# Performance work log

Hardware: AMD Instinct MI355X
Metric: run time of the kernel (lower is better)

## Reference

```python
import jax, jax.numpy as jnp
import numpy as np

BN_EPS = 1e-5


def knn_idx(x, k):
    # x: (B, N, C) -> (B, N, k) indices of k nearest neighbors (incl. self),
    # DGCNN style: topk of negative squared distance.
    inner = jnp.einsum('bnc,bmc->bnm', x, x)
    sq = jnp.sum(x * x, axis=-1)
    neg_dist = 2.0 * inner - sq[:, :, None] - sq[:, None, :]
    _, idx = jax.lax.top_k(neg_dist, k)
    return idx


def edge_conv(x, W, b, gamma, beta, k):
    # x: (B, N, C); W: (O, 2C). One DGCNN EdgeConv block:
    # knn gather -> concat(nbr - x, x) -> conv1x1 -> BN(batch stats) -> GELU -> max over k.
    idx = knn_idx(x, k)                                   # (B, N, k)
    nbr = jax.vmap(lambda f, i: f[i])(x, idx)             # (B, N, k, C)
    ctr = jnp.broadcast_to(x[:, :, None, :], nbr.shape)
    feat = jnp.concatenate([nbr - ctr, ctr], axis=-1)     # (B, N, k, 2C)
    y = jnp.einsum('bnkc,oc->bnko', feat, W) + b          # conv 1x1
    mean = jnp.mean(y, axis=(0, 1, 2))
    var = jnp.var(y, axis=(0, 1, 2))
    y = (y - mean) * jax.lax.rsqrt(var + BN_EPS) * gamma + beta
    y = jax.nn.gelu(y, approximate=False)                 # torch nn.GELU default (erf)
    return jnp.max(y, axis=2)                             # (B, N, O)


def setup_inputs() -> dict:
    key = jax.random.key(0)
    ks = jax.random.split(key, 8)
    bs, ch, n_patches, n_samples = 4, 6, 32, 256
    dims_in = [12, 32, 64, 128, 256]
    dims_out = [16, 32, 64, 128, 256]
    inp = {'x': jax.random.normal(ks[0], (bs, ch, n_patches, n_samples), dtype=jnp.float32)}
    for i, (ci, co) in enumerate(zip(dims_in, dims_out), start=1):
        wk = jax.random.fold_in(ks[1], i)
        scale = 1.0 / np.sqrt(ci)
        inp[f'W{i}'] = (jax.random.normal(wk, (co, ci), dtype=jnp.float32) * scale)
        inp[f'b{i}'] = jnp.zeros((co,), dtype=jnp.float32)
        inp[f'g{i}'] = jnp.ones((co,), dtype=jnp.float32)
        inp[f'bt{i}'] = jnp.zeros((co,), dtype=jnp.float32)
    inp['k'] = 16
    return inp


def reference(x, W1, b1, g1, bt1, W2, b2, g2, bt2, W3, b3, g3, bt3,
              W4, b4, g4, bt4, W5, b5, g5, bt5, k):
    bs, ch, n_patches, n_samples = x.shape
    # (bs, ch, P, S) -> (bs*P, S, ch)  [channels-last point clouds]
    h = x.transpose(0, 2, 3, 1).reshape(bs * n_patches, n_samples, ch)
    h = edge_conv(h, W1, b1, g1, bt1, k)
    h = edge_conv(h, W2, b2, g2, bt2, k)
    h = edge_conv(h, W3, b3, g3, bt3, k)
    h = edge_conv(h, W4, b4, g4, bt4, k)
    h = edge_conv(h, W5, b5, g5, bt5, k)      # (bs*P, S, dim)
    dim = h.shape[-1]
    h = h.reshape(bs, n_patches, n_samples, dim)
    return h.transpose(0, 3, 1, 2)            # (bs, dim, n_patches, n_samples)
```

## Files before the change

kernel.cpp:

```cpp
#include <hip/hip_runtime.h>
#include <cmath>

#define NPTS 256
#define TOTPTS 32768
#define KNB 16

static const size_t OFF_HA   = 0;
static const size_t OFF_HB   = 4194304;
static const size_t OFF_UZ   = 6291456;
static const size_t OFF_YMAX = 23068672;
static const size_t OFF_YMIN = 31457280;
static const size_t OFF_IDX  = 39845888;
static const size_t OFF_VT   = 40370176;
static const size_t OFF_SUMS = 40458240;

__device__ __forceinline__ float gelu_erf(float v) {
  return 0.5f * v * (1.0f + erff(v * 0.70710678118654752f));
}

__global__ __launch_bounds__(256) void prep_kernel(
    const float* __restrict__ x, float* __restrict__ h0,
    const float* __restrict__ W1, const float* __restrict__ W2, const float* __restrict__ W3,
    const float* __restrict__ W4, const float* __restrict__ W5,
    float* __restrict__ Vt, double* __restrict__ sums) {
  const int stride = gridDim.x * blockDim.x;
  const int tid0 = blockIdx.x * blockDim.x + threadIdx.x;
  for (int id = tid0; id < 196608; id += stride) {
    int ch = id % 6;
    int r  = id / 6;
    int s  = r & 255;
    int p  = (r >> 8) & 31;
    int bs = r >> 13;
    h0[id] = x[(((size_t)(bs * 6 + ch) * 32 + p) << 8) + s];
  }
  for (int id = tid0; id < 87232; id += stride) {
    const float* W; int K, N2, base;
    if (id < 192)        { W = W1; K = 6;   N2 = 32;  base = 0; }
    else if (id < 1216)  { W = W2; K = 16;  N2 = 64;  base = 192; }
    else if (id < 5312)  { W = W3; K = 32;  N2 = 128; base = 1216; }
    else if (id < 21696) { W = W4; K = 64;  N2 = 256; base = 5312; }
    else                 { W = W5; K = 128; N2 = 512; base = 21696; }
    int e = id - base;
    int c = e / N2;
    int j = e - c * N2;
    int O = N2 >> 1;
    Vt[id] = (j < O) ? W[j * 2 * K + c] : W[(j - O) * 2 * K + K + c];
  }
  for (int id = tid0; id < 992; id += stride) sums[id] = 0.0;
}

template<int C>
__global__ __launch_bounds__(256) void sq_kernel(const float* __restrict__ h,
                                                 double* __restrict__ sqd) {
  const int n = blockIdx.x * 256 + threadIdx.x;
  const float* p = h + (size_t)n * C;
  double q0 = 0.0, q1 = 0.0;
  #pragma unroll
  for (int c = 0; c + 1 < C; c += 2) {
    q0 = fma((double)p[c],   (double)p[c],   q0);
    q1 = fma((double)p[c+1], (double)p[c+1], q1);
  }
  #pragma unroll
  for (int c = C & ~1; c < C; ++c) q0 = fma((double)p[c], (double)p[c], q0);
  sqd[n] = q0 + q1;
}

template<int K>
__global__ __launch_bounds__(256) void dist_kernel(const float* __restrict__ h,
                                                   const double* __restrict__ sqd,
                                                   double* __restrict__ nd) {
  constexpr int KC = (K < 32) ? K : 32;
  __shared__ __align__(16) float As[KC * 68];
  __shared__ __align__(16) float Bs[KC * 68];
  const int cloud = blockIdx.x >> 4;
  const int tile  = blockIdx.x & 15;
  const int i0 = (tile >> 2) * 64;
  const int j0 = (tile & 3) * 64;
  const float* hb = h + (size_t)cloud * NPTS * K;
  const int tid = threadIdx.x;
  const int mm = (tid & 15) * 4;
  const int jj = (tid >> 4) * 4;
  double acc[4][4] = {{0.0}};
  for (int k0 = 0; k0 < K; k0 += KC) {
    for (int e = tid; e < 64 * KC; e += 256) {
      int am = e / KC, ac = e - am * KC;
      As[ac * 68 + am] = hb[(size_t)(i0 + am) * K + k0 + ac];
    }
    for (int e = tid; e < 64 * KC; e += 256) {
      int bm = e / KC, bc = e - bm * KC;
      Bs[bc * 68 + bm] = hb[(size_t)(j0 + bm) * K + k0 + bc];
    }
    __syncthreads();
    #pragma unroll
    for (int c = 0; c < KC; ++c) {
      float4 av = *(const float4*)(As + c * 68 + mm);
      float4 bv = *(const float4*)(Bs + c * 68 + jj);
      double a0 = (double)av.x, a1 = (double)av.y, a2 = (double)av.z, a3 = (double)av.w;
      double b0 = (double)bv.x, b1 = (double)bv.y, b2 = (double)bv.z, b3 = (double)bv.w;
      acc[0][0] = fma(a0, b0, acc[0][0]);
      acc[0][1] = fma(a0, b1, acc[0][1]);
      acc[0][2] = fma(a0, b2, acc[0][2]);
      acc[0][3] = fma(a0, b3, acc[0][3]);
      acc[1][0] = fma(a1, b0, acc[1][0]);
      acc[1][1] = fma(a1, b1, acc[1][1]);
      acc[1][2] = fma(a1, b2, acc[1][2]);
      acc[1][3] = fma(a1, b3, acc[1][3]);
      acc[2][0] = fma(a2, b0, acc[2][0]);
      acc[2][1] = fma(a2, b1, acc[2][1]);
      acc[2][2] = fma(a2, b2, acc[2][2]);
      acc[2][3] = fma(a2, b3, acc[2][3]);
      acc[3][0] = fma(a3, b0, acc[3][0]);
      acc[3][1] = fma(a3, b1, acc[3][1]);
      acc[3][2] = fma(a3, b2, acc[3][2]);
      acc[3][3] = fma(a3, b3, acc[3][3]);
    }
    __syncthreads();
  }
  double sqi[4], sqj[4];
  #pragma unroll
  for (int r = 0; r < 4; ++r) sqi[r] = sqd[cloud * NPTS + i0 + mm + r];
  #pragma unroll
  for (int s = 0; s < 4; ++s) sqj[s] = sqd[cloud * NPTS + j0 + jj + s];
  double* orow = nd + (size_t)cloud * NPTS * NPTS;
  #pragma unroll
  for (int r = 0; r < 4; ++r) {
    double v0 = 2.0 * acc[r][0] - sqi[r] - sqj[0];
    double v1 = 2.0 * acc[r][1] - sqi[r] - sqj[1];
    double v2 = 2.0 * acc[r][2] - sqi[r] - sqj[2];
    double v3 = 2.0 * acc[r][3] - sqi[r] - sqj[3];
    double* p = orow + (size_t)(i0 + mm + r) * NPTS + j0 + jj;
    *(double2*)(p)     = make_double2(v0, v1);
    *(double2*)(p + 2) = make_double2(v2, v3);
  }
}

__global__ __launch_bounds__(256) void topk_merge2_kernel(const double* __restrict__ nd,
                                                          int* __restrict__ idxout) {
  const unsigned long long FULL = 0xFFFFFFFFFFFFFFFFull;
  const int wid  = threadIdx.x >> 6;
  const int lane = threadIdx.x & 63;
  const int half = lane >> 5;
  const int sub  = lane & 31;
  const int rowAB = blockIdx.x * 16 + wid * 4 + half;
  const int rowCD = blockIdx.x * 16 + wid * 4 + 2 + half;
  const double* rp1 = nd + (size_t)rowAB * NPTS + 8 * sub;
  const double* rp2 = nd + (size_t)rowCD * NPTS + 8 * sub;
  const unsigned cb = 8u * (unsigned)sub;

  #define MK(P, Q) ((((unsigned long long)__double_as_longlong(P)) & ~0xFFull) | (cb + (Q)))
  double2 t0 = *(const double2*)(rp1);
  double2 t1 = *(const double2*)(rp1 + 2);
  double2 t2 = *(const double2*)(rp1 + 4);
  double2 t3 = *(const double2*)(rp1 + 6);
  unsigned long long a0 = MK(t0.x, 0u), a1 = MK(t0.y, 1u), a2 = MK(t1.x, 2u), a3 = MK(t1.y, 3u);
  unsigned long long a4 = MK(t2.x, 4u), a5 = MK(t2.y, 5u), a6 = MK(t3.x, 6u), a7 = MK(t3.y, 7u);
  t0 = *(const double2*)(rp2);
  t1 = *(const double2*)(rp2 + 2);
  t2 = *(const double2*)(rp2 + 4);
  t3 = *(const double2*)(rp2 + 6);
  unsigned long long b0 = MK(t0.x, 0u), b1 = MK(t0.y, 1u), b2 = MK(t1.x, 2u), b3 = MK(t1.y, 3u);
  unsigned long long b4 = MK(t2.x, 4u), b5 = MK(t2.y, 5u), b6 = MK(t3.x, 6u), b7 = MK(t3.y, 7u);
  #undef MK

  #define CE(X, Y) { unsigned long long lo_ = (X < Y) ? X : Y; \
                     unsigned long long hi_ = (X < Y) ? Y : X; X = lo_; Y = hi_; }
  #define SORT8(v0,v1,v2,v3,v4,v5,v6,v7) \
    CE(v0,v1) CE(v2,v3) CE(v4,v5) CE(v6,v7) \
    CE(v0,v2) CE(v1,v3) CE(v4,v6) CE(v5,v7) \
    CE(v1,v2) CE(v5,v6) \
    CE(v0,v4) CE(v1,v5) CE(v2,v6) CE(v3,v7) \
    CE(v2,v4) CE(v3,v5) \
    CE(v1,v2) CE(v3,v4) CE(v5,v6)
  SORT8(a0,a1,a2,a3,a4,a5,a6,a7)
  SORT8(b0,b1,b2,b3,b4,b5,b6,b7)
  #undef SORT8
  #undef CE

  int keep1 = 0, keep2 = 0;
  for (int round = 0; round < KNB; ++round) {
    unsigned long long m1 = a0, m2 = b0, o;
    o = __shfl_xor(m1, 16); m1 = (o < m1) ? o : m1;
    o = __shfl_xor(m2, 16); m2 = (o < m2) ? o : m2;
    o = __shfl_xor(m1, 8);  m1 = (o < m1) ? o : m1;
    o = __shfl_xor(m2, 8);  m2 = (o < m2) ? o : m2;
    o = __shfl_xor(m1, 4);  m1 = (o < m1) ? o : m1;
    o = __shfl_xor(m2, 4);  m2 = (o < m2) ? o : m2;
    o = __shfl_xor(m1, 2);  m1 = (o < m1) ? o : m1;
    o = __shfl_xor(m2, 2);  m2 = (o < m2) ? o : m2;
    o = __shfl_xor(m1, 1);  m1 = (o < m1) ? o : m1;
    o = __shfl_xor(m2, 1);  m2 = (o < m2) ? o : m2;
    const int col1 = (int)(m1 & 0xFFull);
    const int col2 = (int)(m2 & 0xFFull);
    if ((col1 >> 3) == sub) {
      a0 = a1; a1 = a2; a2 = a3; a3 = a4; a4 = a5; a5 = a6; a6 = a7; a7 = FULL;
    }
    if ((col2 >> 3) == sub) {
      b0 = b1; b1 = b2; b2 = b3; b3 = b4; b4 = b5; b5 = b6; b6 = b7; b7 = FULL;
    }
    if (sub == round) { keep1 = col1; keep2 = col2; }
  }
  if (sub < KNB) {
    idxout[(size_t)rowAB * KNB + sub] = (rowAB & ~(NPTS - 1)) + keep1;
    idxout[(size_t)rowCD * KNB + sub] = (rowCD & ~(NPTS - 1)) + keep2;
  }
}

template<int K, int N2>
__global__ __launch_bounds__(256) void gemm_uz_kernel(const float* __restrict__ h,
                                                      const float* __restrict__ Vt,
                                                      float* __restrict__ UZ) {
  constexpr int KC = 32;
  constexpr int NBLK = (N2 + 63) / 64;
  __shared__ __align__(16) float As[KC * 68];
  __shared__ __align__(16) float Bs[KC * 68];
  const int m0 = (int)(blockIdx.x / NBLK) * 64;
  const int n0 = (int)(blockIdx.x % NBLK) * 64;
  const int tid = threadIdx.x;
  const int mm = (tid & 15) * 4;
  const int jj = (tid >> 4) * 4;
  float acc[4][4] = {{0.f}};
  for (int k0 = 0; k0 < K; k0 += KC) {
    #pragma unroll
    for (int e = tid; e < 64 * KC; e += 256) {
      int am = e / KC, ac = e - am * KC;
      float v = 0.f;
      if (k0 + ac < K) v = h[(size_t)(m0 + am) * K + k0 + ac];
      As[ac * 68 + am] = v;
    }
    #pragma unroll
    for (int e = tid; e < KC * 64; e += 256) {
      int bj = e & 63, bc = e >> 6;
      float v = 0.f;
      if (k0 + bc < K && n0 + bj < N2) v = Vt[(size_t)(k0 + bc) * N2 + n0 + bj];
      Bs[bc * 68 + bj] = v;
    }
    __syncthreads();
    #pragma unroll
    for (int c = 0; c < KC; ++c) {
      float4 av = *(const float4*)(As + c * 68 + mm);
      float4 bv = *(const float4*)(Bs + c * 68 + jj);
      acc[0][0] = fmaf(av.x, bv.x, acc[0][0]);
      acc[0][1] = fmaf(av.x, bv.y, acc[0][1]);
      acc[0][2] = fmaf(av.x, bv.z, acc[0][2]);
      acc[0][3] = fmaf(av.x, bv.w, acc[0][3]);
      acc[1][0] = fmaf(av.y, bv.x, acc[1][0]);
      acc[1][1] = fmaf(av.y, bv.y, acc[1][1]);
      acc[1][2] = fmaf(av.y, bv.z, acc[1][2]);
      acc[1][3] = fmaf(av.y, bv.w, acc[1][3]);
      acc[2][0] = fmaf(av.z, bv.x, acc[2][0]);
      acc[2][1] = fmaf(av.z, bv.y, acc[2][1]);
      acc[2][2] = fmaf(av.z, bv.z, acc[2][2]);
      acc[2][3] = fmaf(av.z, bv.w, acc[2][3]);
      acc[3][0] = fmaf(av.w, bv.x, acc[3][0]);
      acc[3][1] = fmaf(av.w, bv.y, acc[3][1]);
      acc[3][2] = fmaf(av.w, bv.z, acc[3][2]);
      acc[3][3] = fmaf(av.w, bv.w, acc[3][3]);
    }
    __syncthreads();
  }
  if (n0 + jj < N2) {
    #pragma unroll
    for (int i = 0; i < 4; ++i) {
      float4 v = make_float4(acc[i][0], acc[i][1], acc[i][2], acc[i][3]);
      *(float4*)(UZ + (size_t)(m0 + mm + i) * N2 + n0 + jj) = v;
    }
  }
}

template<int K, int N2>
__global__ __launch_bounds__(256) void gemm_big_kernel(const float* __restrict__ h,
                                                       const float* __restrict__ Vt,
                                                       float* __restrict__ UZ) {
  constexpr int KC = 32;
  constexpr int PAD = 132;
  constexpr int NBLK = N2 / 128;
  __shared__ __align__(16) float As[KC * PAD];
  __shared__ __align__(16) float Bs[KC * PAD];
  const int m0 = (int)(blockIdx.x / NBLK) * 128;
  const int n0 = (int)(blockIdx.x % NBLK) * 128;
  const int tid = threadIdx.x;
  const int ra = (tid & 15) * 4;
  const int ca = (tid >> 4) * 4;
  float acc[8][8];
  #pragma unroll
  for (int i = 0; i < 8; ++i)
    #pragma unroll
    for (int j = 0; j < 8; ++j) acc[i][j] = 0.f;

  for (int k0 = 0; k0 < K; k0 += KC) {
    #pragma unroll
    for (int q = 0; q < 4; ++q) {
      int idx = tid + 256 * q;
      int am = idx >> 3;
      int aq = idx & 7;
      float4 v = *(const float4*)(h + (size_t)(m0 + am) * K + k0 + 4 * aq);
      As[(4 * aq + 0) * PAD + am] = v.x;
      As[(4 * aq + 1) * PAD + am] = v.y;
      As[(4 * aq + 2) * PAD + am] = v.z;
      As[(4 * aq + 3) * PAD + am] = v.w;
    }
    #pragma unroll
    for (int q = 0; q < 4; ++q) {
      int idx = tid + 256 * q;
      int bk = idx >> 5;
      int bq = idx & 31;
      *(float4*)(Bs + bk * PAD + 4 * bq) =
          *(const float4*)(Vt + (size_t)(k0 + bk) * N2 + n0 + 4 * bq);
    }
    __syncthreads();
    #pragma unroll
    for (int cc = 0; cc < KC; ++cc) {
      float4 a0 = *(const float4*)(As + cc * PAD + ra);
      float4 a1 = *(const float4*)(As + cc * PAD + 64 + ra);
      float4 b0 = *(const float4*)(Bs + cc * PAD + ca);
      float4 b1 = *(const float4*)(Bs + cc * PAD + 64 + ca);
      float av[8] = {a0.x, a0.y, a0.z, a0.w, a1.x, a1.y, a1.z, a1.w};
      float bv[8] = {b0.x, b0.y, b0.z, b0.w, b1.x, b1.y, b1.z, b1.w};
      #pragma unroll
      for (int i = 0; i < 8; ++i)
        #pragma unroll
        for (int j = 0; j < 8; ++j)
          acc[i][j] = fmaf(av[i], bv[j], acc[i][j]);
    }
    __syncthreads();
  }
  #pragma unroll
  for (int i = 0; i < 8; ++i) {
    int row = m0 + ((i < 4) ? (ra + i) : (64 + ra + (i - 4)));
    float4 v0 = make_float4(acc[i][0], acc[i][1], acc[i][2], acc[i][3]);
    float4 v1 = make_float4(acc[i][4], acc[i][5], acc[i][6], acc[i][7]);
    *(float4*)(UZ + (size_t)row * N2 + n0 + ca) = v0;
    *(float4*)(UZ + (size_t)row * N2 + n0 + 64 + ca) = v1;
  }
}

template<int O, int GRID>
__global__ __launch_bounds__(256) void combine_kernel(const float* __restrict__ UZ,
    const int* __restrict__ idx, const float* __restrict__ bias,
    float* __restrict__ ymax, float* __restrict__ ymin, double* __restrict__ partials) {
  constexpr int TPP = O / 4;
  constexpr int PPI = 256 / TPP;
  constexpr int PPB = TOTPTS / GRID;
  constexpr int ITERS = PPB / PPI;
  static_assert(ITERS >= 1, "grid too large for this O");
  constexpr int BPC = GRID / 128;
  __shared__ double red[256];
  const int tid = threadIdx.x;
  const int oc  = tid % TPP;
  const int sub = tid / TPP;
  const int x    = blockIdx.x & 7;
  const int slot = blockIdx.x >> 3;
  const int c    = x + 8 * (slot / BPC);
  const int w    = slot % BPC;
  const int base = c * NPTS + w * PPB;
  const float4* UZ4 = (const float4*)UZ;
  float4* ymx4 = (float4*)ymax;
  float4* ymn4 = (float4*)ymin;
  const float4 b4 = ((const float4*)bias)[oc];
  double a1x = 0.0, a1y = 0.0, a1z = 0.0, a1w = 0.0;
  double a2x = 0.0, a2y = 0.0, a2z = 0.0, a2w = 0.0;
  for (int it = 0; it < ITERS; ++it) {
    int n = base + it * PPI + sub;
    const int* ip = idx + (size_t)n * KNB;
    float4 un = UZ4[(size_t)n * (O / 2) + oc];
    float4 zn = UZ4[(size_t)n * (O / 2) + O / 4 + oc];
    float4 w4 = make_float4(zn.x - un.x + b4.x, zn.y - un.y + b4.y,
                            zn.z - un.z + b4.z, zn.w - un.w + b4.w);
    float4 mx = make_float4(-INFINITY, -INFINITY, -INFINITY, -INFINITY);
    float4 mn = make_float4(INFINITY, INFINITY, INFINITY, INFINITY);
    float4 s1 = make_float4(0.f, 0.f, 0.f, 0.f);
    float4 s2 = make_float4(0.f, 0.f, 0.f, 0.f);
    #pragma unroll
    for (int kk = 0; kk < KNB; ++kk) {
      int j = ip[kk];
      float4 uv = UZ4[(size_t)j * (O / 2) + oc];
      mx.x = fmaxf(mx.x, uv.x); mx.y = fmaxf(mx.y, uv.y);
      mx.z = fmaxf(mx.z, uv.z); mx.w = fmaxf(mx.w, uv.w);
      mn.x = fminf(mn.x, uv.x); mn.y = fminf(mn.y, uv.y);
      mn.z = fminf(mn.z, uv.z); mn.w = fminf(mn.w, uv.w);
      s1.x += uv.x; s1.y += uv.y; s1.z += uv.z; s1.w += uv.w;
      s2.x = fmaf(uv.x, uv.x, s2.x); s2.y = fmaf(uv.y, uv.y, s2.y);
      s2.z = fmaf(uv.z, uv.z, s2.z); s2.w = fmaf(uv.w, uv.w, s2.w);
    }
    ymx4[(size_t)n * (O / 4) + oc] = make_float4(mx.x + w4.x, mx.y + w4.y, mx.z + w4.z, mx.w + w4.w);
    ymn4[(size_t)n * (O / 4) + oc] = make_float4(mn.x + w4.x, mn.y + w4.y, mn.z + w4.z, mn.w + w4.w);
    a1x += (double)(s1.x + 16.f * w4.x);
    a1y += (double)(s1.y + 16.f * w4.y);
    a1z += (double)(s1.z + 16.f * w4.z);
    a1w += (double)(s1.w + 16.f * w4.w);
    a2x += (double)(s2.x + 2.f * w4.x * s1.x + 16.f * (w4.x * w4.x));
    a2y += (double)(s2.y + 2.f * w4.y * s1.y + 16.f * (w4.y * w4.y));
    a2z += (double)(s2.z + 2.f * w4.z * s1.z + 16.f * (w4.z * w4.z));
    a2w += (double)(s2.w + 2.f * w4.w * s1.w + 16.f * (w4.w * w4.w));
  }
  #define REDUCE_ONE(VAL, CH_OFF)                                        \
    red[tid] = (VAL);                                                    \
    __syncthreads();                                                     \
    if (tid < TPP) {                                                     \
      double t = 0.0;                                                    \
      _Pragma("unroll")                                                  \
      for (int q = 0; q < PPI; ++q) t += red[q * TPP + tid];             \
      partials[(size_t)((CH_OFF) + 4 * tid) * GRID + blockIdx.x] = t;    \
    }                                                                    \
    __syncthreads();
  REDUCE_ONE(a1x, 0)
  REDUCE_ONE(a1y, 1)
  REDUCE_ONE(a1z, 2)
  REDUCE_ONE(a1w, 3)
  REDUCE_ONE(a2x, O + 0)
  REDUCE_ONE(a2y, O + 1)
  REDUCE_ONE(a2z, O + 2)
  REDUCE_ONE(a2w, O + 3)
  #undef REDUCE_ONE
}

template<int NB>
__global__ __launch_bounds__(256) void reduce_sums_kernel(const double* __restrict__ part,
                                                          double* __restrict__ sums) {
  __shared__ double red[256];
  const int ch = blockIdx.x;
  const double* p = part + (size_t)ch * NB;
  double t = 0.0;
  for (int i = threadIdx.x; i < NB; i += 256) t += p[i];
  red[threadIdx.x] = t;
  __syncthreads();
  #pragma unroll
  for (int s = 128; s > 0; s >>= 1) {
    if (threadIdx.x < s) red[threadIdx.x] += red[threadIdx.x + s];
    __syncthreads();
  }
  if (threadIdx.x == 0) sums[ch] = red[0];
}

template<int O>
__global__ __launch_bounds__(256) void apply_kernel(const float* __restrict__ ymax,
    const float* __restrict__ ymin, const double* __restrict__ sums,
    const float* __restrict__ g, const float* __restrict__ bt, float* __restrict__ hout) {
  const int tid = blockIdx.x * 256 + threadIdx.x;
  const int o = tid & (O - 1);
  double m = sums[o] * (1.0 / 524288.0);
  double v = fma(-m, m, sums[O + o] * (1.0 / 524288.0));
  float A = g[o] / sqrtf((float)v + 1e-5f);
  float Cc = fmaf(-(float)m, A, bt[o]);
  float r1 = gelu_erf(fmaf(A, ymax[tid], Cc));
  float r2 = gelu_erf(fmaf(A, ymin[tid], Cc));
  hout[tid] = fmaxf(r1, r2);
}

__global__ __launch_bounds__(256) void apply_final_kernel(const float* __restrict__ ymax,
    const float* __restrict__ ymin, const double* __restrict__ sums,
    const float* __restrict__ g, const float* __restrict__ bt, float* __restrict__ out) {
  constexpr int O = 256;
  __shared__ float tile[64 * 65];
  const int bo = blockIdx.x & 3;
  const int bn = blockIdx.x >> 2;
  const int n0 = bn * 64, o0 = bo * 64;
  const int lane = threadIdx.x & 63;
  const int grp = threadIdx.x >> 6;
  {
    const int oc = o0 + lane;
    double m = sums[oc] * (1.0 / 524288.0);
    double v = fma(-m, m, sums[O + oc] * (1.0 / 524288.0));
    float A = g[oc] / sqrtf((float)v + 1e-5f);
    float Cc = fmaf(-(float)m, A, bt[oc]);
    #pragma unroll
    for (int q = 0; q < 16; ++q) {
      int r = grp * 16 + q;
      size_t src = (size_t)(n0 + r) * O + oc;
      float r1 = gelu_erf(fmaf(A, ymax[src], Cc));
      float r2 = gelu_erf(fmaf(A, ymin[src], Cc));
      tile[r * 65 + lane] = fmaxf(r1, r2);
    }
  }
  __syncthreads();
  const int s0 = n0 & 255;
  const int p  = (n0 >> 8) & 31;
  const int bs = n0 >> 13;
  size_t basei = ((size_t)(bs * 256 + o0) * 32 + p) * 256 + s0;
  #pragma unroll
  for (int q = 0; q < 16; ++q) {
    int c = grp * 16 + q;
    out[basei + (size_t)c * 8192 + lane] = tile[lane * 65 + c];
  }
}

extern "C" void kernel_launch(void* const* d_in, const int* in_sizes, int n_in,
                              void* d_out, int out_size, void* d_ws, size_t ws_size,
                              hipStream_t stream) {
  (void)in_sizes; (void)n_in; (void)out_size; (void)ws_size;
  const float* x   = (const float*)d_in[0];
  const float* W1  = (const float*)d_in[1];
  const float* b1  = (const float*)d_in[2];
  const float* g1  = (const float*)d_in[3];
  const float* bt1 = (const float*)d_in[4];
  const float* W2  = (const float*)d_in[5];
  const float* b2  = (const float*)d_in[6];
  const float* g2  = (const float*)d_in[7];
  const float* bt2 = (const float*)d_in[8];
  const float* W3  = (const float*)d_in[9];
  const float* b3  = (const float*)d_in[10];
  const float* g3  = (const float*)d_in[11];
  const float* bt3 = (const float*)d_in[12];
  const float* W4  = (const float*)d_in[13];
  const float* b4  = (const float*)d_in[14];
  const float* g4  = (const float*)d_in[15];
  const float* bt4 = (const float*)d_in[16];
  const float* W5  = (const float*)d_in[17];
  const float* b5  = (const float*)d_in[18];
  const float* g5  = (const float*)d_in[19];
  const float* bt5 = (const float*)d_in[20];

  float* ws    = (float*)d_ws;
  float* hA    = ws + OFF_HA;
  float* hB    = ws + OFF_HB;
  float* UZ    = ws + OFF_UZ;
  float* ymx   = ws + OFF_YMAX;
  float* ymn   = ws + OFF_YMIN;
  int*   idxb  = (int*)(ws + OFF_IDX);
  float* Vt    = ws + OFF_VT;
  double* sums = (double*)(ws + OFF_SUMS);
  double* nd   = (double*)UZ;
  double* sqd  = (double*)ymx;
  double* partA = (double*)hA;
  double* partB = (double*)hB;

  prep_kernel<<<256, 256, 0, stream>>>(x, hA, W1, W2, W3, W4, W5, Vt, sums);

  sq_kernel<6><<<128, 256, 0, stream>>>(hA, sqd);
  dist_kernel<6><<<2048, 256, 0, stream>>>(hA, sqd, nd);
  topk_merge2_kernel<<<2048, 256, 0, stream>>>(nd, idxb);
  gemm_uz_kernel<6, 32><<<512, 256, 0, stream>>>(hA, Vt + 0, UZ);
  combine_kernel<16, 512><<<512, 256, 0, stream>>>(UZ, idxb, b1, ymx, ymn, partA);
  reduce_sums_kernel<512><<<32, 256, 0, stream>>>(partA, sums + 0);
  apply_kernel<16><<<2048, 256, 0, stream>>>(ymx, ymn, sums + 0, g1, bt1, hB);

  sq_kernel<16><<<128, 256, 0, stream>>>(hB, sqd);
  dist_kernel<16><<<2048, 256, 0, stream>>>(hB, sqd, nd);
  topk_merge2_kernel<<<2048, 256, 0, stream>>>(nd, idxb);
  gemm_uz_kernel<16, 64><<<512, 256, 0, stream>>>(hB, Vt + 192, UZ);
  combine_kernel<32, 1024><<<1024, 256, 0, stream>>>(UZ, idxb, b2, ymx, ymn, partB);
  reduce_sums_kernel<1024><<<64, 256, 0, stream>>>(partB, sums + 32);
  apply_kernel<32><<<4096, 256, 0, stream>>>(ymx, ymn, sums + 32, g2, bt2, hA);

  sq_kernel<32><<<128, 256, 0, stream>>>(hA, sqd);
  dist_kernel<32><<<2048, 256, 0, stream>>>(hA, sqd, nd);
  topk_merge2_kernel<<<2048, 256, 0, stream>>>(nd, idxb);
  gemm_big_kernel<32, 128><<<256, 256, 0, stream>>>(hA, Vt + 1216, UZ);
  combine_kernel<64, 2048><<<2048, 256, 0, stream>>>(UZ, idxb, b3, ymx, ymn, partA);
  reduce_sums_kernel<2048><<<128, 256, 0, stream>>>(partA, sums + 96);
  apply_kernel<64><<<8192, 256, 0, stream>>>(ymx, ymn, sums + 96, g3, bt3, hB);

  sq_kernel<64><<<128, 256, 0, stream>>>(hB, sqd);
  dist_kernel<64><<<2048, 256, 0, stream>>>(hB, sqd, nd);
  topk_merge2_kernel<<<2048, 256, 0, stream>>>(nd, idxb);
  gemm_big_kernel<64, 256><<<512, 256, 0, stream>>>(hB, Vt + 5312, UZ);
  combine_kernel<128, 2048><<<2048, 256, 0, stream>>>(UZ, idxb, b4, ymx, ymn, partB);
  reduce_sums_kernel<2048><<<256, 256, 0, stream>>>(partB, sums + 224);
  apply_kernel<128><<<16384, 256, 0, stream>>>(ymx, ymn, sums + 224, g4, bt4, hA);

  sq_kernel<128><<<128, 256, 0, stream>>>(hA, sqd);
  dist_kernel<128><<<2048, 256, 0, stream>>>(hA, sqd, nd);
  topk_merge2_kernel<<<2048, 256, 0, stream>>>(nd, idxb);
  gemm_big_kernel<128, 512><<<1024, 256, 0, stream>>>(hA, Vt + 21696, UZ);
  combine_kernel<256, 2048><<<2048, 256, 0, stream>>>(UZ, idxb, b5, ymx, ymn, partA);
  reduce_sums_kernel<2048><<<512, 256, 0, stream>>>(partA, sums + 480);
  apply_final_kernel<<<2048, 256, 0, stream>>>(ymx, ymn, sums + 480, g5, bt5, (float*)d_out);
}
```

Baseline: 708.4 us.

## Fuse pairwise-distance GEMM with top-k selection in shared memory

Merges the distance kernel and the top-k kernel into one kernel per layer. Each block computes 32 rows by all 256 columns of the negative distance matrix in fp64, packs the keys into shared memory and runs the existing warp-shuffle top-16 selection from there. This removes the write and re-read of the 256x256 fp64 distance matrix per cloud through global memory, plus one launch per layer. In exchange it uses about 66KB of shared memory per block, which limits occupancy, and the column tile is reloaded twice per block.

```diff
diff --git a/kernel.cpp b/kernel.cpp
--- a/kernel.cpp
+++ b/kernel.cpp
@@ -66,142 +66,137 @@
 }
 
 template<int K>
-__global__ __launch_bounds__(256) void dist_kernel(const float* __restrict__ h,
-                                                   const double* __restrict__ sqd,
-                                                   double* __restrict__ nd) {
-  constexpr int KC = (K < 32) ? K : 32;
-  __shared__ __align__(16) float As[KC * 68];
-  __shared__ __align__(16) float Bs[KC * 68];
-  const int cloud = blockIdx.x >> 4;
-  const int tile  = blockIdx.x & 15;
-  const int i0 = (tile >> 2) * 64;
-  const int j0 = (tile & 3) * 64;
+__global__ __launch_bounds__(256) void knn_fused_kernel(const float* __restrict__ h,
+                                                        const double* __restrict__ sqd,
+                                                        int* __restrict__ idxout) {
+  constexpr int KC = (K < 16) ? K : 16;
+  __shared__ unsigned long long keys[32 * 257];
+  __shared__ __align__(16) float As[KC * 36];
+  __shared__ __align__(16) float Bs[KC * 132];
+  const int cloud = blockIdx.x >> 3;
+  const int i0 = (blockIdx.x & 7) * 32;
   const float* hb = h + (size_t)cloud * NPTS * K;
   const int tid = threadIdx.x;
-  const int mm = (tid & 15) * 4;
-  const int jj = (tid >> 4) * 4;
-  double acc[4][4] = {{0.0}};
-  for (int k0 = 0; k0 < K; k0 += KC) {
-    for (int e = tid; e < 64 * KC; e += 256) {
-      int am = e / KC, ac = e - am * KC;
-      As[ac * 68 + am] = hb[(size_t)(i0 + am) * K + k0 + ac];
-    }
-    for (int e = tid; e < 64 * KC; e += 256) {
-      int bm = e / KC, bc = e - bm * KC;
-      Bs[bc * 68 + bm] = hb[(size_t)(j0 + bm) * K + k0 + bc];
-    }
-    __syncthreads();
-    #pragma unroll
-    for (int c = 0; c < KC; ++c) {
-      float4 av = *(const float4*)(As + c * 68 + mm);
-      float4 bv = *(const float4*)(Bs + c * 68 + jj);
-      double a0 = (double)av.x, a1 = (double)av.y, a2 = (double)av.z, a3 = (double)av.w;
-      double b0 = (double)bv.x, b1 = (double)bv.y, b2 = (double)bv.z, b3 = (double)bv.w;
-      acc[0][0] = fma(a0, b0, acc[0][0]);
-      acc[0][1] = fma(a0, b1, acc[0][1]);
-      acc[0][2] = fma(a0, b2, acc[0][2]);
-      acc[0][3] = fma(a0, b3, acc[0][3]);
-      acc[1][0] = fma(a1, b0, acc[1][0]);
-      acc[1][1] = fma(a1, b1, acc[1][1]);
-      acc[1][2] = fma(a1, b2, acc[1][2]);
-      acc[1][3] = fma(a1, b3, acc[1][3]);
-      acc[2][0] = fma(a2, b0, acc[2][0]);
-      acc[2][1] = fma(a2, b1, acc[2][1]);
-      acc[2][2] = fma(a2, b2, acc[2][2]);
-      acc[2][3] = fma(a2, b3, acc[2][3]);
-      acc[3][0] = fma(a3, b0, acc[3][0]);
-      acc[3][1] = fma(a3, b1, acc[3][1]);
-      acc[3][2] = fma(a3, b2, acc[3][2]);
-      acc[3][3] = fma(a3, b3, acc[3][3]);
-    }
-    __syncthreads();
-  }
-  double sqi[4], sqj[4];
+  const int mm = (tid & 7) * 4;
+  const int jj = (tid >> 3) * 4;
+
+  double sqi[4];
   #pragma unroll
   for (int r = 0; r < 4; ++r) sqi[r] = sqd[cloud * NPTS + i0 + mm + r];
-  #pragma unroll
-  for (int s = 0; s < 4; ++s) sqj[s] = sqd[cloud * NPTS + j0 + jj + s];
-  double* orow = nd + (size_t)cloud * NPTS * NPTS;
-  #pragma unroll
-  for (int r = 0; r < 4; ++r) {
-    double v0 = 2.0 * acc[r][0] - sqi[r] - sqj[0];
-    double v1 = 2.0 * acc[r][1] - sqi[r] - sqj[1];
-    double v2 = 2.0 * acc[r][2] - sqi[r] - sqj[2];
-    double v3 = 2.0 * acc[r][3] - sqi[r] - sqj[3];
-    double* p = orow + (size_t)(i0 + mm + r) * NPTS + j0 + jj;
-    *(double2*)(p)     = make_double2(v0, v1);
-    *(double2*)(p + 2) = make_double2(v2, v3);
-  }
-}
-
-__global__ __launch_bounds__(256) void topk_merge2_kernel(const double* __restrict__ nd,
-                                                          int* __restrict__ idxout) {
+
+  for (int jh = 0; jh < 2; ++jh) {
+    const int j0 = jh * 128;
+    double acc[4][4] = {{0.0}};
+    for (int k0 = 0; k0 < K; k0 += KC) {
+      for (int e = tid; e < 32 * KC; e += 256) {
+        int am = e / KC, ac = e - am * KC;
+        As[ac * 36 + am] = hb[(size_t)(i0 + am) * K + k0 + ac];
+      }
+      for (int e = tid; e < 128 * KC; e += 256) {
+        int bm = e / KC, bc = e - bm * KC;
+        Bs[bc * 132 + bm] = hb[(size_t)(j0 + bm) * K + k0 + bc];
+      }
+      __syncthreads();
+      #pragma unroll
+      for (int c = 0; c < KC; ++c) {
+        float4 av = *(const float4*)(As + c * 36 + mm);
+        float4 bv = *(const float4*)(Bs + c * 132 + jj);
+        double a0 = (double)av.x, a1 = (double)av.y, a2 = (double)av.z, a3 = (double)av.w;
+        double b0 = (double)bv.x, b1 = (double)bv.y, b2 = (double)bv.z, b3 = (double)bv.w;
+        acc[0][0] = fma(a0, b0, acc[0][0]);
+        acc[0][1] = fma(a0, b1, acc[0][1]);
+        acc[0][2] = fma(a0, b2, acc[0][2]);
+        acc[0][3] = fma(a0, b3, acc[0][3]);
+        acc[1][0] = fma(a1, b0, acc[1][0]);
+        acc[1][1] = fma(a1, b1, acc[1][1]);
+        acc[1][2] = fma(a1, b2, acc[1][2]);
+        acc[1][3] = fma(a1, b3, acc[1][3]);
+        acc[2][0] = fma(a2, b0, acc[2][0]);
+        acc[2][1] = fma(a2, b1, acc[2][1]);
+        acc[2][2] = fma(a2, b2, acc[2][2]);
+        acc[2][3] = fma(a2, b3, acc[2][3]);
+        acc[3][0] = fma(a3, b0, acc[3][0]);
+        acc[3][1] = fma(a3, b1, acc[3][1]);
+        acc[3][2] = fma(a3, b2, acc[3][2]);
+        acc[3][3] = fma(a3, b3, acc[3][3]);
+      }
+      __syncthreads();
+    }
+    double sqj[4];
+    #pragma unroll
+    for (int s = 0; s < 4; ++s) sqj[s] = sqd[cloud * NPTS + j0 + jj + s];
+    #pragma unroll
+    for (int r = 0; r < 4; ++r) {
+      #pragma unroll
+      for (int s = 0; s < 4; ++s) {
+        double v = 2.0 * acc[r][s] - sqi[r] - sqj[s];
+        int col = j0 + jj + s;
+        keys[(mm + r) * 257 + col] =
+            (((unsigned long long)__double_as_longlong(v)) & ~0xFFull) |
+            (unsigned long long)col;
+      }
+    }
+  }
+  __syncthreads();
+
   const unsigned long long FULL = 0xFFFFFFFFFFFFFFFFull;
-  const int wid  = threadIdx.x >> 6;
-  const int lane = threadIdx.x & 63;
+  const int wid  = tid >> 6;
+  const int lane = tid & 63;
   const int half = lane >> 5;
   const int sub  = lane & 31;
-  const int rowAB = blockIdx.x * 16 + wid * 4 + half;
-  const int rowCD = blockIdx.x * 16 + wid * 4 + 2 + half;
-  const double* rp1 = nd + (size_t)rowAB * NPTS + 8 * sub;
-  const double* rp2 = nd + (size_t)rowCD * NPTS + 8 * sub;
-  const unsigned cb = 8u * (unsigned)sub;
-
-  #define MK(P, Q) ((((unsigned long long)__double_as_longlong(P)) & ~0xFFull) | (cb + (Q)))
-  double2 t0 = *(const double2*)(rp1);
-  double2 t1 = *(const double2*)(rp1 + 2);
-  double2 t2 = *(const double2*)(rp1 + 4);
-  double2 t3 = *(const double2*)(rp1 + 6);
-  unsigned long long a0 = MK(t0.x, 0u), a1 = MK(t0.y, 1u), a2 = MK(t1.x, 2u), a3 = MK(t1.y, 3u);
-  unsigned long long a4 = MK(t2.x, 4u), a5 = MK(t2.y, 5u), a6 = MK(t3.x, 6u), a7 = MK(t3.y, 7u);
-  t0 = *(const double2*)(rp2);
-  t1 = *(const double2*)(rp2 + 2);
-  t2 = *(const double2*)(rp2 + 4);
-  t3 = *(const double2*)(rp2 + 6);
-  unsigned long long b0 = MK(t0.x, 0u), b1 = MK(t0.y, 1u), b2 = MK(t1.x, 2u), b3 = MK(t1.y, 3u);
-  unsigned long long b4 = MK(t2.x, 4u), b5 = MK(t2.y, 5u), b6 = MK(t3.x, 6u), b7 = MK(t3.y, 7u);
-  #undef MK
-
-  #define CE(X, Y) { unsigned long long lo_ = (X < Y) ? X : Y; \
-                     unsigned long long hi_ = (X < Y) ? Y : X; X = lo_; Y = hi_; }
-  #define SORT8(v0,v1,v2,v3,v4,v5,v6,v7) \
-    CE(v0,v1) CE(v2,v3) CE(v4,v5) CE(v6,v7) \
-    CE(v0,v2) CE(v1,v3) CE(v4,v6) CE(v5,v7) \
-    CE(v1,v2) CE(v5,v6) \
-    CE(v0,v4) CE(v1,v5) CE(v2,v6) CE(v3,v7) \
-    CE(v2,v4) CE(v3,v5) \
-    CE(v1,v2) CE(v3,v4) CE(v5,v6)
-  SORT8(a0,a1,a2,a3,a4,a5,a6,a7)
-  SORT8(b0,b1,b2,b3,b4,b5,b6,b7)
-  #undef SORT8
-  #undef CE
-
-  int keep1 = 0, keep2 = 0;
-  for (int round = 0; round < KNB; ++round) {
-    unsigned long long m1 = a0, m2 = b0, o;
-    o = __shfl_xor(m1, 16); m1 = (o < m1) ? o : m1;
-    o = __shfl_xor(m2, 16); m2 = (o < m2) ? o : m2;
-    o = __shfl_xor(m1, 8);  m1 = (o < m1) ? o : m1;
-    o = __shfl_xor(m2, 8);  m2 = (o < m2) ? o : m2;
-    o = __shfl_xor(m1, 4);  m1 = (o < m1) ? o : m1;
-    o = __shfl_xor(m2, 4);  m2 = (o < m2) ? o : m2;
-    o = __shfl_xor(m1, 2);  m1 = (o < m1) ? o : m1;
-    o = __shfl_xor(m2, 2);  m2 = (o < m2) ? o : m2;
-    o = __shfl_xor(m1, 1);  m1 = (o < m1) ? o : m1;
-    o = __shfl_xor(m2, 1);  m2 = (o < m2) ? o : m2;
-    const int col1 = (int)(m1 & 0xFFull);
-    const int col2 = (int)(m2 & 0xFFull);
-    if ((col1 >> 3) == sub) {
-      a0 = a1; a1 = a2; a2 = a3; a3 = a4; a4 = a5; a5 = a6; a6 = a7; a7 = FULL;
-    }
-    if ((col2 >> 3) == sub) {
-      b0 = b1; b1 = b2; b2 = b3; b3 = b4; b4 = b5; b5 = b6; b6 = b7; b7 = FULL;
-    }
-    if (sub == round) { keep1 = col1; keep2 = col2; }
-  }
-  if (sub < KNB) {
-    idxout[(size_t)rowAB * KNB + sub] = (rowAB & ~(NPTS - 1)) + keep1;
-    idxout[(size_t)rowCD * KNB + sub] = (rowCD & ~(NPTS - 1)) + keep2;
+  for (int p = 0; p < 2; ++p) {
+    const int rA = p * 16 + wid * 4 + half;
+    const int rC = rA + 2;
+    const unsigned long long* rp1 = keys + rA * 257 + 8 * sub;
+    const unsigned long long* rp2 = keys + rC * 257 + 8 * sub;
+    unsigned long long a0 = rp1[0], a1 = rp1[1], a2 = rp1[2], a3 = rp1[3];
+    unsigned long long a4 = rp1[4], a5 = rp1[5], a6 = rp1[6], a7 = rp1[7];
+    unsigned long long b0 = rp2[0], b1 = rp2[1], b2 = rp2[2], b3 = rp2[3];
+    unsigned long long b4 = rp2[4], b5 = rp2[5], b6 = rp2[6], b7 = rp2[7];
+
+    #define CE(X, Y) { unsigned long long lo_ = (X < Y) ? X : Y; \
+                       unsigned long long hi_ = (X < Y) ? Y : X; X = lo_; Y = hi_; }
+    #define SORT8(v0,v1,v2,v3,v4,v5,v6,v7) \
+      CE(v0,v1) CE(v2,v3) CE(v4,v5) CE(v6,v7) \
+      CE(v0,v2) CE(v1,v3) CE(v4,v6) CE(v5,v7) \
+      CE(v1,v2) CE(v5,v6) \
+      CE(v0,v4) CE(v1,v5) CE(v2,v6) CE(v3,v7) \
+      CE(v2,v4) CE(v3,v5) \
+      CE(v1,v2) CE(v3,v4) CE(v5,v6)
+    SORT8(a0,a1,a2,a3,a4,a5,a6,a7)
+    SORT8(b0,b1,b2,b3,b4,b5,b6,b7)
+    #undef SORT8
+    #undef CE
+
+    int keep1 = 0, keep2 = 0;
+    for (int round = 0; round < KNB; ++round) {
+      unsigned long long m1 = a0, m2 = b0, o;
+      o = __shfl_xor(m1, 16); m1 = (o < m1) ? o : m1;
+      o = __shfl_xor(m2, 16); m2 = (o < m2) ? o : m2;
+      o = __shfl_xor(m1, 8);  m1 = (o < m1) ? o : m1;
+      o = __shfl_xor(m2, 8);  m2 = (o < m2) ? o : m2;
+      o = __shfl_xor(m1, 4);  m1 = (o < m1) ? o : m1;
+      o = __shfl_xor(m2, 4);  m2 = (o < m2) ? o : m2;
+      o = __shfl_xor(m1, 2);  m1 = (o < m1) ? o : m1;
+      o = __shfl_xor(m2, 2);  m2 = (o < m2) ? o : m2;
+      o = __shfl_xor(m1, 1);  m1 = (o < m1) ? o : m1;
+      o = __shfl_xor(m2, 1);  m2 = (o < m2) ? o : m2;
+      const int col1 = (int)(m1 & 0xFFull);
+      const int col2 = (int)(m2 & 0xFFull);
+      if ((col1 >> 3) == sub) {
+        a0 = a1; a1 = a2; a2 = a3; a3 = a4; a4 = a5; a5 = a6; a6 = a7; a7 = FULL;
+      }
+      if ((col2 >> 3) == sub) {
+        b0 = b1; b1 = b2; b2 = b3; b3 = b4; b4 = b5; b5 = b6; b6 = b7; b7 = FULL;
+      }
+      if (sub == round) { keep1 = col1; keep2 = col2; }
+    }
+    if (sub < KNB) {
+      const int growA = cloud * NPTS + i0 + rA;
+      const int growC = cloud * NPTS + i0 + rC;
+      idxout[(size_t)growA * KNB + sub] = cloud * NPTS + keep1;
+      idxout[(size_t)growC * KNB + sub] = cloud * NPTS + keep2;
+    }
   }
 }
 
@@ -519,7 +514,6 @@
   int*   idxb  = (int*)(ws + OFF_IDX);
   float* Vt    = ws + OFF_VT;
   double* sums = (double*)(ws + OFF_SUMS);
-  double* nd   = (double*)UZ;
   double* sqd  = (double*)ymx;
   double* partA = (double*)hA;
   double* partB = (double*)hB;
@@ -527,40 +521,35 @@
   prep_kernel<<<256, 256, 0, stream>>>(x, hA, W1, W2, W3, W4, W5, Vt, sums);
 
   sq_kernel<6><<<128, 256, 0, stream>>>(hA, sqd);
-  dist_kernel<6><<<2048, 256, 0, stream>>>(hA, sqd, nd);
-  topk_merge2_kernel<<<2048, 256, 0, stream>>>(nd, idxb);
+  knn_fused_kernel<6><<<1024, 256, 0, stream>>>(hA, sqd, idxb);
   gemm_uz_kernel<6, 32><<<512, 256, 0, stream>>>(hA, Vt + 0, UZ);
   combine_kernel<16, 512><<<512, 256, 0, stream>>>(UZ, idxb, b1, ymx, ymn, partA);
   reduce_sums_kernel<512><<<32, 256, 0, stream>>>(partA, sums + 0);
   apply_kernel<16><<<2048, 256, 0, stream>>>(ymx, ymn, sums + 0, g1, bt1, hB);
 
   sq_kernel<16><<<128, 256, 0, stream>>>(hB, sqd);
-  dist_kernel<16><<<2048, 256, 0, stream>>>(hB, sqd, nd);
-  topk_merge2_kernel<<<2048, 256, 0, stream>>>(nd, idxb);
+  knn_fused_kernel<16><<<1024, 256, 0, stream>>>(hB, sqd, idxb);
   gemm_uz_kernel<16, 64><<<512, 256, 0, stream>>>(hB, Vt + 192, UZ);
   combine_kernel<32, 1024><<<1024, 256, 0, stream>>>(UZ, idxb, b2, ymx, ymn, partB);
   reduce_sums_kernel<1024><<<64, 256, 0, stream>>>(partB, sums + 32);
   apply_kernel<32><<<4096, 256, 0, stream>>>(ymx, ymn, sums + 32, g2, bt2, hA);
 
   sq_kernel<32><<<128, 256, 0, stream>>>(hA, sqd);
-  dist_kernel<32><<<2048, 256, 0, stream>>>(hA, sqd, nd);
-  topk_merge2_kernel<<<2048, 256, 0, stream>>>(nd, idxb);
+  knn_fused_kernel<32><<<1024, 256, 0, stream>>>(hA, sqd, idxb);
   gemm_big_kernel<32, 128><<<256, 256, 0, stream>>>(hA, Vt + 1216, UZ);
   combine_kernel<64, 2048><<<2048, 256, 0, stream>>>(UZ, idxb, b3, ymx, ymn, partA);
   reduce_sums_kernel<2048><<<128, 256, 0, stream>>>(partA, sums + 96);
   apply_kernel<64><<<8192, 256, 0, stream>>>(ymx, ymn, sums + 96, g3, bt3, hB);
 
   sq_kernel<64><<<128, 256, 0, stream>>>(hB, sqd);
-  dist_kernel<64><<<2048, 256, 0, stream>>>(hB, sqd, nd);
-  topk_merge2_kernel<<<2048, 256, 0, stream>>>(nd, idxb);
+  knn_fused_kernel<64><<<1024, 256, 0, stream>>>(hB, sqd, idxb);
   gemm_big_kernel<64, 256><<<512, 256, 0, stream>>>(hB, Vt + 5312, UZ);
   combine_kernel<128, 2048><<<2048, 256, 0, stream>>>(UZ, idxb, b4, ymx, ymn, partB);
   reduce_sums_kernel<2048><<<256, 256, 0, stream>>>(partB, sums + 224);
   apply_kernel<128><<<16384, 256, 0, stream>>>(ymx, ymn, sums + 224, g4, bt4, hA);
 
   sq_kernel<128><<<128, 256, 0, stream>>>(hA, sqd);
-  dist_kernel<128><<<2048, 256, 0, stream>>>(hA, sqd, nd);
-  topk_merge2_kernel<<<2048, 256, 0, stream>>>(nd, idxb);
+  knn_fused_kernel<128><<<1024, 256, 0, stream>>>(hA, sqd, idxb);
   gemm_big_kernel<128, 512><<<1024, 256, 0, stream>>>(hA, Vt + 21696, UZ);
   combine_kernel<256, 2048><<<2048, 256, 0, stream>>>(UZ, idxb, b5, ymx, ymn, partA);
   reduce_sums_kernel<2048><<<512, 256, 0, stream>>>(partA, sums + 480);
```

Measured after the change: 784.7 us. +10.8%, slower.

## Exploit distance symmetry and overlap per-layer GEMM with kNN on a second stream

Applied to the files above, without the earlier changes.

The distance kernel now computes only the upper-triangular 64x64 tiles of each cloud's 256x256 distance matrix (10 of 16 tiles) and mirrors the off-diagonal tiles by writing them transposed. Blocks are mapped so that consecutive block IDs go to different XCDs. Each layer's UZ GEMM now runs on a second stream, overlapping the sq/dist/top-k chain and joined with events before combine. Buffers are reassigned so that the concurrent kernels do not alias: nd goes into the ymx region and the sq buffers into the free h buffer. The trade-offs are uncoalesced transposed stores, event overhead, and correctness that depends on buffer lifetimes and on the static second stream.

```diff
diff --git a/kernel.cpp b/kernel.cpp
--- a/kernel.cpp
+++ b/kernel.cpp
@@ -66,16 +66,20 @@
 }
 
 template<int K>
-__global__ __launch_bounds__(256) void dist_kernel(const float* __restrict__ h,
-                                                   const double* __restrict__ sqd,
-                                                   double* __restrict__ nd) {
+__global__ __launch_bounds__(256) void dist_sym_kernel(const float* __restrict__ h,
+                                                       const double* __restrict__ sqd,
+                                                       double* __restrict__ nd) {
   constexpr int KC = (K < 32) ? K : 32;
   __shared__ __align__(16) float As[KC * 68];
   __shared__ __align__(16) float Bs[KC * 68];
-  const int cloud = blockIdx.x >> 4;
-  const int tile  = blockIdx.x & 15;
-  const int i0 = (tile >> 2) * 64;
-  const int j0 = (tile & 3) * 64;
+  const int xcd  = blockIdx.x & 7;
+  const int t    = blockIdx.x >> 3;
+  const int cloud = xcd + 8 * (t / 10);
+  const int p    = t % 10;
+  const int ti   = (p < 4) ? 0 : ((p < 7) ? 1 : ((p < 9) ? 2 : 3));
+  const int tj   = p - ((ti == 0) ? 0 : ((ti == 1) ? 3 : ((ti == 2) ? 5 : 6)));
+  const int i0 = ti * 64;
+  const int j0 = tj * 64;
   const float* hb = h + (size_t)cloud * NPTS * K;
   const int tid = threadIdx.x;
   const int mm = (tid & 15) * 4;
@@ -128,9 +132,21 @@
     double v1 = 2.0 * acc[r][1] - sqi[r] - sqj[1];
     double v2 = 2.0 * acc[r][2] - sqi[r] - sqj[2];
     double v3 = 2.0 * acc[r][3] - sqi[r] - sqj[3];
-    double* p = orow + (size_t)(i0 + mm + r) * NPTS + j0 + jj;
-    *(double2*)(p)     = make_double2(v0, v1);
-    *(double2*)(p + 2) = make_double2(v2, v3);
+    double* pw = orow + (size_t)(i0 + mm + r) * NPTS + j0 + jj;
+    *(double2*)(pw)     = make_double2(v0, v1);
+    *(double2*)(pw + 2) = make_double2(v2, v3);
+  }
+  if (i0 != j0) {
+    #pragma unroll
+    for (int s = 0; s < 4; ++s) {
+      double m0 = 2.0 * acc[0][s] - sqj[s] - sqi[0];
+      double m1 = 2.0 * acc[1][s] - sqj[s] - sqi[1];
+      double m2 = 2.0 * acc[2][s] - sqj[s] - sqi[2];
+      double m3 = 2.0 * acc[3][s] - sqj[s] - sqi[3];
+      double* pT = orow + (size_t)(j0 + jj + s) * NPTS + i0 + mm;
+      *(double2*)(pT)     = make_double2(m0, m1);
+      *(double2*)(pT + 2) = make_double2(m2, m3);
+    }
   }
 }
 
@@ -519,50 +535,77 @@
   int*   idxb  = (int*)(ws + OFF_IDX);
   float* Vt    = ws + OFF_VT;
   double* sums = (double*)(ws + OFF_SUMS);
-  double* nd   = (double*)UZ;
-  double* sqd  = (double*)ymx;
+  double* nd   = (double*)ymx;
+  double* sqA  = (double*)hA;
+  double* sqB  = (double*)hB;
   double* partA = (double*)hA;
   double* partB = (double*)hB;
 
+  static hipStream_t s2 = nullptr;
+  static hipEvent_t evF[5], evJ[5];
+  if (s2 == nullptr) {
+    hipStreamCreateWithFlags(&s2, hipStreamNonBlocking);
+    for (int i = 0; i < 5; ++i) {
+      hipEventCreateWithFlags(&evF[i], hipEventDisableTiming);
+      hipEventCreateWithFlags(&evJ[i], hipEventDisableTiming);
+    }
+  }
+
+  #define FORK(l)  hipEventRecord(evF[l], stream); hipStreamWaitEvent(s2, evF[l], 0);
+  #define JOIN(l)  hipEventRecord(evJ[l], s2);     hipStreamWaitEvent(stream, evJ[l], 0);
+
   prep_kernel<<<256, 256, 0, stream>>>(x, hA, W1, W2, W3, W4, W5, Vt, sums);
 
-  sq_kernel<6><<<128, 256, 0, stream>>>(hA, sqd);
-  dist_kernel<6><<<2048, 256, 0, stream>>>(hA, sqd, nd);
+  FORK(0)
+  gemm_uz_kernel<6, 32><<<512, 256, 0, s2>>>(hA, Vt + 0, UZ);
+  sq_kernel<6><<<128, 256, 0, stream>>>(hA, sqB);
+  dist_sym_kernel<6><<<1280, 256, 0, stream>>>(hA, sqB, nd);
   topk_merge2_kernel<<<2048, 256, 0, stream>>>(nd, idxb);
-  gemm_uz_kernel<6, 32><<<512, 256, 0, stream>>>(hA, Vt + 0, UZ);
+  JOIN(0)
   combine_kernel<16, 512><<<512, 256, 0, stream>>>(UZ, idxb, b1, ymx, ymn, partA);
   reduce_sums_kernel<512><<<32, 256, 0, stream>>>(partA, sums + 0);
   apply_kernel<16><<<2048, 256, 0, stream>>>(ymx, ymn, sums + 0, g1, bt1, hB);
 
-  sq_kernel<16><<<128, 256, 0, stream>>>(hB, sqd);
-  dist_kernel<16><<<2048, 256, 0, stream>>>(hB, sqd, nd);
+  FORK(1)
+  gemm_uz_kernel<16, 64><<<512, 256, 0, s2>>>(hB, Vt + 192, UZ);
+  sq_kernel<16><<<128, 256, 0, stream>>>(hB, sqA);
+  dist_sym_kernel<16><<<1280, 256, 0, stream>>>(hB, sqA, nd);
   topk_merge2_kernel<<<2048, 256, 0, stream>>>(nd, idxb);
-  gemm_uz_kernel<16, 64><<<512, 256, 0, stream>>>(hB, Vt + 192, UZ);
+  JOIN(1)
   combine_kernel<32, 1024><<<1024, 256, 0, stream>>>(UZ, idxb, b2, ymx, ymn, partB);
   reduce_sums_kernel<1024><<<64, 256, 0, stream>>>(partB, sums + 32);
   apply_kernel<32><<<4096, 256, 0, stream>>>(ymx, ymn, sums + 32, g2, bt2, hA);
 
-  sq_kernel<32><<<128, 256, 0, stream>>>(hA, sqd);
-  dist_kernel<32><<<2048, 256, 0, stream>>>(hA, sqd, nd);
+  FORK(2)
+  gemm_big_kernel<32, 128><<<256, 256, 0, s2>>>(hA, Vt + 1216, UZ);
+  sq_kernel<32><<<128, 256, 0, stream>>>(hA, sqB);
+  dist_sym_kernel<32><<<1280, 256, 0, stream>>>(hA, sqB, nd);
   topk_merge2_kernel<<<2048, 256, 0, stream>>>(nd, idxb);
-  gemm_big_kernel<32, 128><<<256, 256, 0, stream>>>(hA, Vt + 1216, UZ);
+  JOIN(2)
   combine_kernel<64, 2048><<<2048, 256, 0, stream>>>(UZ, idxb, b3, ymx, ymn, partA);
   reduce_sums_kernel<2048><<<128, 256, 0, stream>>>(partA, sums + 96);
   apply_kernel<64><<<8192, 256, 0, stream>>>(ymx, ymn, sums + 96, g3, bt3, hB);
 
-  sq_kernel<64><<<128, 256, 0, stream>>>(hB, sqd);
-  dist_kernel<64><<<2048, 256, 0, stream>>>(hB, sqd, nd);
+  FORK(3)
+  gemm_big_kernel<64, 256><<<512, 256, 0, s2>>>(hB, Vt + 5312, UZ);
+  sq_kernel<64><<<128, 256, 0, stream>>>(hB, sqA);
+  dist_sym_kernel<64><<<1280, 256, 0, stream>>>(hB, sqA, nd);
   topk_merge2_kernel<<<2048, 256, 0, stream>>>(nd, idxb);
-  gemm_big_kernel<64, 256><<<512, 256, 0, stream>>>(hB, Vt + 5312, UZ);
+  JOIN(3)
   combine_kernel<128, 2048><<<2048, 256, 0, stream>>>(UZ, idxb, b4, ymx, ymn, partB);
   reduce_sums_kernel<2048><<<256, 256, 0, stream>>>(partB, sums + 224);
   apply_kernel<128><<<16384, 256, 0, stream>>>(ymx, ymn, sums + 224, g4, bt4, hA);
 
-  sq_kernel<128><<<128, 256, 0, stream>>>(hA, sqd);
-  dist_kernel<128><<<2048, 256, 0, stream>>>(hA, sqd, nd);
+  FORK(4)
+  gemm_big_kernel<128, 512><<<1024, 256, 0, s2>>>(hA, Vt + 21696, UZ);
+  sq_kernel<128><<<128, 256, 0, stream>>>(hA, sqB);
+  dist_sym_kernel<128><<<1280, 256, 0, stream>>>(hA, sqB, nd);
   topk_merge2_kernel<<<2048, 256, 0, stream>>>(nd, idxb);
-  gemm_big_kernel<128, 512><<<1024, 256, 0, stream>>>(hA, Vt + 21696, UZ);
+  JOIN(4)
   combine_kernel<256, 2048><<<2048, 256, 0, stream>>>(UZ, idxb, b5, ymx, ymn, partA);
   reduce_sums_kernel<2048><<<512, 256, 0, stream>>>(partA, sums + 480);
   apply_final_kernel<<<2048, 256, 0, stream>>>(ymx, ymn, sums + 480, g5, bt5, (float*)d_out);
-}
+
+  #undef FORK
+  #undef JOIN
+}
```

Result: slower. 735.5 us (+3.8%).
